# Optimization experiments

Measured on AMD Instinct MI355X. Metric: run time of the kernel, lower is better.

The kernel has to match this reference:

```python
import jax, jax.numpy as jnp
import numpy as np

N_HEAD = 16
NEG_BIG = 1e10

def setup_inputs() -> dict:
    key = jax.random.key(0)
    k1, k2, k3 = jax.random.split(key, 3)
    B, S, D = 2, 2048, 1024
    x = jax.random.normal(k1, (B, S, D), dtype=jnp.float32)
    c_attn_w = jax.random.normal(k2, (D, 3 * D), dtype=jnp.float32) * 0.02
    c_attn_b = jnp.zeros((3 * D,), dtype=jnp.float32)
    c_proj_w = jax.random.normal(k3, (D, D), dtype=jnp.float32) * 0.02
    c_proj_b = jnp.zeros((D,), dtype=jnp.float32)
    return {"x": x, "c_attn_w": c_attn_w, "c_attn_b": c_attn_b,
            "c_proj_w": c_proj_w, "c_proj_b": c_proj_b}

def reference(x, c_attn_w, c_attn_b, c_proj_w, c_proj_b):
    B, S, D = x.shape
    H = N_HEAD
    hd = D // H
    # Conv1D c_attn: x @ W + b -> (B, S, 3D)
    qkv = x @ c_attn_w + c_attn_b
    q, k, v = jnp.split(qkv, 3, axis=-1)
    # split heads -> (B, H, S, hd)
    q = q.reshape(B, S, H, hd).transpose(0, 2, 1, 3)
    k = k.reshape(B, S, H, hd).transpose(0, 2, 1, 3)
    v = v.reshape(B, S, H, hd).transpose(0, 2, 1, 3)
    # QK^T with scale (scale=True)
    w = jnp.einsum('bhqd,bhkd->bhqk', q, k) / jnp.sqrt(jnp.float32(hd))
    # additive/multiplicative causal mask, exactly as source: w*b - 1e10*(1-b)
    b = jnp.tril(jnp.ones((S, S), dtype=w.dtype))
    w = w * b - NEG_BIG * (1.0 - b)
    w = jax.nn.softmax(w, axis=-1)
    a = jnp.einsum('bhqk,bhkd->bhqd', w, v)
    # merge heads -> (B, S, D)
    a = a.transpose(0, 2, 1, 3).reshape(B, S, D)
    # Conv1D c_proj
    a = a @ c_proj_w + c_proj_b
    # present = stack(key (as (B,H,S,hd)), value)
    present = jnp.stack((k, v))
    return (a, present)
```

## Files before the change

### kernel.cpp

```cpp
#include <hip/hip_runtime.h>
#include <hip/hip_bf16.h>
#include <string.h>

#define BB 2
#define SS 2048
#define DD 1024
#define NH 16
#define TT (BB * SS)
#define N3 (3 * DD)
#define A_SIZE (TT * DD)
#define PRESENT_HALF (BB * NH * SS * 64)
#define C2Q 0.18033688011112043f

typedef __attribute__((ext_vector_type(8))) short short8;
typedef __attribute__((ext_vector_type(4))) float floatx4;
typedef __attribute__((ext_vector_type(8))) unsigned short ushort8;

__device__ __forceinline__ unsigned short f2bf(float f) {
    union { float f; unsigned u; } v; v.f = f;
    unsigned r = v.u + 0x7fffu + ((v.u >> 16) & 1u);
    return (unsigned short)(r >> 16);
}
__device__ __forceinline__ unsigned pack2bf(float a, float b) {
    __hip_bfloat162 h = __float22bfloat162_rn(float2{a, b});
    unsigned u; memcpy(&u, &h, 4); return u;
}
__device__ __forceinline__ float bf2f(unsigned short u) {
    union { unsigned u; float f; } v; v.u = ((unsigned)u) << 16; return v.f;
}

__device__ __forceinline__ void async16(const unsigned short* g, unsigned short* lds) {
    __builtin_amdgcn_global_load_lds(
        (const __attribute__((address_space(1))) unsigned int*)g,
        (__attribute__((address_space(3))) unsigned int*)lds,
        16, 0, 0);
}

__global__ __launch_bounds__(256) void cast_x_kernel(const float* __restrict__ src,
                                                     unsigned short* __restrict__ dst) {
    int i = (blockIdx.x * 256 + threadIdx.x) * 8;
    float4 a = *(const float4*)(src + i);
    float4 b = *(const float4*)(src + i + 4);
    ushort8 o;
    o[0] = f2bf(a.x); o[1] = f2bf(a.y); o[2] = f2bf(a.z); o[3] = f2bf(a.w);
    o[4] = f2bf(b.x); o[5] = f2bf(b.y); o[6] = f2bf(b.z); o[7] = f2bf(b.w);
    *(ushort8*)(dst + i) = o;
}

__global__ __launch_bounds__(256) void transpose_cast_kernel(const float* __restrict__ src,
                                                             unsigned short* __restrict__ dst,
                                                             int R, int C) {
    __shared__ float tile[32][33];
    int c0 = blockIdx.x * 32, r0 = blockIdx.y * 32;
    int tx = threadIdx.x, ty = threadIdx.y;
    for (int i = ty; i < 32; i += 8)
        tile[i][tx] = src[(size_t)(r0 + i) * C + c0 + tx];
    __syncthreads();
    for (int i = ty; i < 32; i += 8)
        dst[(size_t)(c0 + i) * R + r0 + tx] = f2bf(tile[tx][i]);
}

__global__ __launch_bounds__(256)
void vtrans_kernel(const unsigned short* __restrict__ qkv,
                   unsigned short* __restrict__ vT) {
    __shared__ unsigned short tile[64][72];
    int bh = blockIdx.x, st = blockIdx.y;
    int b = bh >> 4, h = bh & 15;
    int tid = threadIdx.x;
    int r = tid >> 2, c = (tid & 3) * 16;
    const unsigned short* src = qkv + ((size_t)(b * SS + st * 64 + r)) * 3072 + 2048 + h * 64 + c;
    *(int4*)(&tile[r][c])     = *(const int4*)(src);
    *(int4*)(&tile[r][c + 8]) = *(const int4*)(src + 8);
    __syncthreads();
    int d = tid >> 2, s0 = (tid & 3) * 16;
    unsigned short tmp[16];
    for (int e = 0; e < 16; ++e) tmp[e] = tile[s0 + e][d];
    unsigned short* dst = vT + ((size_t)bh * 64 + d) * SS + st * 64 + s0;
    *(int4*)(dst)     = *(const int4*)(tmp);
    *(int4*)(dst + 8) = *(const int4*)(tmp + 8);
}

__global__ __launch_bounds__(256)
void present_kernel(const unsigned short* __restrict__ qkvb, float* __restrict__ out) {
    size_t e = ((size_t)blockIdx.x * 256 + threadIdx.x) * 8;
    int d = (int)(e & 63);
    int s = (int)((e >> 6) & 2047);
    int h = (int)((e >> 17) & 15);
    int b = (int)((e >> 21) & 1);
    int half = (int)(e >> 22);
    const unsigned short* src = qkvb + ((size_t)(b * SS + s)) * 3072 + 1024 + half * 1024 + h * 64 + d;
    ushort8 u = *(const ushort8*)src;
    float* dst = out + A_SIZE + e;
    float4 f0 = {bf2f(u[0]), bf2f(u[1]), bf2f(u[2]), bf2f(u[3])};
    float4 f1 = {bf2f(u[4]), bf2f(u[5]), bf2f(u[6]), bf2f(u[7])};
    *(float4*)(dst) = f0;
    *(float4*)(dst + 4) = f1;
}

__global__ __launch_bounds__(256)
void gemm_kernel(const unsigned short* __restrict__ A,
                 const unsigned short* __restrict__ Bt,
                 const float* __restrict__ bias,
                 int mode,
                 unsigned short* __restrict__ out_bf,
                 float* __restrict__ out_f) {
    __shared__ unsigned short As[2][128][32];
    __shared__ unsigned short Bs[2][128][32];
    const int tid  = threadIdx.x;
    const int t0   = blockIdx.y * 128;
    const int n0   = blockIdx.x * 128;
    const int wave = tid >> 6, lane = tid & 63;
    const int wm = wave >> 1, wn = wave & 1;
    const int l15 = lane & 15, quad = lane >> 4;

    const int sr = lane >> 2;
    const int sc = (lane & 3) * 8;

    floatx4 acc[4][4];
    for (int i = 0; i < 4; ++i)
        for (int j = 0; j < 4; ++j)
            for (int e = 0; e < 4; ++e) acc[i][j][e] = 0.f;

    const unsigned short* gA = A  + (size_t)(t0 + wave * 32 + sr) * 1024 + sc;
    const unsigned short* gB = Bt + (size_t)(n0 + wave * 32 + sr) * 1024 + sc;

    async16(gA,             &As[0][wave * 32][0]);
    async16(gA + 16 * 1024, &As[0][wave * 32 + 16][0]);
    async16(gB,             &Bs[0][wave * 32][0]);
    async16(gB + 16 * 1024, &Bs[0][wave * 32 + 16][0]);

    for (int kt = 0; kt < 32; ++kt) {
        const int cur = kt & 1;
        __syncthreads();
        if (kt < 31) {
            const int k1 = (kt + 1) * 32;
            async16(gA + k1,             &As[cur ^ 1][wave * 32][0]);
            async16(gA + k1 + 16 * 1024, &As[cur ^ 1][wave * 32 + 16][0]);
            async16(gB + k1,             &Bs[cur ^ 1][wave * 32][0]);
            async16(gB + k1 + 16 * 1024, &Bs[cur ^ 1][wave * 32 + 16][0]);
        }
        short8 af[4], bfr[4];
        for (int mt = 0; mt < 4; ++mt)
            af[mt] = *(const short8*)(&As[cur][wm * 64 + mt * 16 + l15][quad * 8]);
        for (int nt = 0; nt < 4; ++nt)
            bfr[nt] = *(const short8*)(&Bs[cur][wn * 64 + nt * 16 + l15][quad * 8]);
        for (int mt = 0; mt < 4; ++mt)
            for (int nt = 0; nt < 4; ++nt)
                acc[mt][nt] = __builtin_amdgcn_mfma_f32_16x16x32_bf16(bfr[nt], af[mt], acc[mt][nt], 0, 0, 0);
    }

    const float qs = (mode == 0 && n0 < 1024) ? C2Q : 1.0f;
    for (int mt = 0; mt < 4; ++mt) {
        const int t = t0 + wm * 64 + mt * 16 + l15;
        if (mode == 0) {
            unsigned short* po = out_bf + (size_t)t * 3072 + n0 + wn * 64;
            for (int nt = 0; nt < 4; ++nt) {
                float4 b4 = *(const float4*)(bias + n0 + wn * 64 + nt * 16 + quad * 4);
                float v0 = (acc[mt][nt][0] + b4.x) * qs;
                float v1 = (acc[mt][nt][1] + b4.y) * qs;
                float v2 = (acc[mt][nt][2] + b4.z) * qs;
                float v3 = (acc[mt][nt][3] + b4.w) * qs;
                uint2 w = {pack2bf(v0, v1), pack2bf(v2, v3)};
                *(uint2*)(po + nt * 16 + quad * 4) = w;
            }
        } else {
            float* po = out_f + (size_t)t * 1024 + n0 + wn * 64;
            for (int nt = 0; nt < 4; ++nt) {
                float4 b4 = *(const float4*)(bias + n0 + wn * 64 + nt * 16 + quad * 4);
                float4 v = {acc[mt][nt][0] + b4.x, acc[mt][nt][1] + b4.y,
                            acc[mt][nt][2] + b4.z, acc[mt][nt][3] + b4.w};
                *(float4*)(po + nt * 16 + quad * 4) = v;
            }
        }
    }
}

__global__ __launch_bounds__(256)
void flash_kernel(const unsigned short* __restrict__ qkv,
                  const unsigned short* __restrict__ vT,
                  unsigned short* __restrict__ out) {
    __shared__ unsigned short Kt[2][64][72];
    __shared__ unsigned short Vt[2][64][72];
    __shared__ unsigned short Pt[4][16][72];

    const int bh = blockIdx.x;
    const int qt = 31 - blockIdx.y;
    const int b = bh >> 4, h = bh & 15;
    const int tid = threadIdx.x;
    const int wave = tid >> 6, lane = tid & 63;
    const int l15 = lane & 15, quad = lane >> 4;

    const size_t rowb = (size_t)b * SS;
    const int kcol = 1024 + h * 64;

    short8 bq0, bq1;
    {
        const unsigned short* qp = qkv + (rowb + qt * 64 + wave * 16 + l15) * 3072 + h * 64 + quad * 8;
        bq0 = *(const short8*)(qp);
        bq1 = *(const short8*)(qp + 32);
    }

    float l_i = 0.f;
    floatx4 o[4];
    for (int dt = 0; dt < 4; ++dt)
        for (int e = 0; e < 4; ++e) o[dt][e] = 0.f;

    const int qrow_l = wave * 16 + l15;

    const int rr = tid >> 3, seg = (tid & 7) * 8;
    const int vr = tid >> 2, vc = (tid & 3) * 16;
    const unsigned short* kb = qkv + rowb * 3072 + kcol;
    const unsigned short* vb = vT + (size_t)bh * 64 * SS;
    int4 ka0, ka1, va0, va1;

    #define PREF(j) { \
        const unsigned short* ks = kb + (size_t)((j) * 64 + rr) * 3072 + seg; \
        ka0 = *(const int4*)(ks); \
        ka1 = *(const int4*)(ks + 32 * 3072); \
        const unsigned short* vs = vb + (size_t)vr * SS + (j) * 64 + vc; \
        va0 = *(const int4*)(vs); \
        va1 = *(const int4*)(vs + 8); }
    #define STAGE(bf_) { \
        *(int4*)(&Kt[bf_][rr][seg])      = ka0; \
        *(int4*)(&Kt[bf_][rr + 32][seg]) = ka1; \
        *(int4*)(&Vt[bf_][vr][vc])       = va0; \
        *(int4*)(&Vt[bf_][vr][vc + 8])   = va1; }

    PREF(0);
    STAGE(0);
    if (qt > 0) PREF(1);

    for (int j = 0; j <= qt; ++j) {
        const int cur = j & 1;
        __syncthreads();
        if (j < qt) {
            STAGE(cur ^ 1);
            if (j + 2 <= qt) PREF(j + 2);
        }

        floatx4 sc[4];
        for (int nt = 0; nt < 4; ++nt)
            for (int e = 0; e < 4; ++e) sc[nt][e] = 0.f;
        for (int nt = 0; nt < 4; ++nt) {
            const unsigned short* kp = &Kt[cur][nt * 16 + l15][quad * 8];
            short8 ak0 = *(const short8*)(kp);
            short8 ak1 = *(const short8*)(kp + 32);
            sc[nt] = __builtin_amdgcn_mfma_f32_16x16x32_bf16(ak0, bq0, sc[nt], 0, 0, 0);
            sc[nt] = __builtin_amdgcn_mfma_f32_16x16x32_bf16(ak1, bq1, sc[nt], 0, 0, 0);
        }
        if (j == qt) {
            for (int nt = 0; nt < 4; ++nt)
                for (int r = 0; r < 4; ++r)
                    if (nt * 16 + quad * 4 + r > qrow_l) sc[nt][r] = -1.0e30f;
        }

        for (int nt = 0; nt < 4; ++nt)
            for (int r = 0; r < 4; ++r) {
                float p = __builtin_amdgcn_exp2f(sc[nt][r]);
                sc[nt][r] = p;
                l_i += p;
            }

        for (int nt = 0; nt < 4; ++nt) {
            uint2 w = {pack2bf(sc[nt][0], sc[nt][1]), pack2bf(sc[nt][2], sc[nt][3])};
            *(uint2*)(&Pt[wave][l15][nt * 16 + quad * 4]) = w;
        }
        asm volatile("s_waitcnt lgkmcnt(0)" ::: "memory");
        short8 bp0 = *(const short8*)(&Pt[wave][l15][quad * 8]);
        short8 bp1 = *(const short8*)(&Pt[wave][l15][32 + quad * 8]);
        for (int dt = 0; dt < 4; ++dt) {
            const unsigned short* vp = &Vt[cur][dt * 16 + l15][quad * 8];
            short8 av0 = *(const short8*)(vp);
            short8 av1 = *(const short8*)(vp + 32);
            o[dt] = __builtin_amdgcn_mfma_f32_16x16x32_bf16(av0, bp0, o[dt], 0, 0, 0);
            o[dt] = __builtin_amdgcn_mfma_f32_16x16x32_bf16(av1, bp1, o[dt], 0, 0, 0);
        }
    }
    #undef PREF
    #undef STAGE

    l_i += __shfl_xor(l_i, 16);
    l_i += __shfl_xor(l_i, 32);
    float inv = 1.f / l_i;
    const int qrow = qt * 64 + wave * 16 + l15;
    unsigned short* po = out + (rowb + qrow) * 1024 + h * 64;
    for (int dt = 0; dt < 4; ++dt) {
        uint2 w = {pack2bf(o[dt][0] * inv, o[dt][1] * inv),
                   pack2bf(o[dt][2] * inv, o[dt][3] * inv)};
        *(uint2*)(po + dt * 16 + quad * 4) = w;
    }
}

extern "C" void kernel_launch(void* const* d_in, const int* in_sizes, int n_in,
                              void* d_out, int out_size, void* d_ws, size_t ws_size,
                              hipStream_t stream) {
    const float* x        = (const float*)d_in[0];
    const float* c_attn_w = (const float*)d_in[1];
    const float* c_attn_b = (const float*)d_in[2];
    const float* c_proj_w = (const float*)d_in[3];
    const float* c_proj_b = (const float*)d_in[4];
    float* out = (float*)d_out;

    char* ws = (char*)d_ws;
    unsigned short* xb     = (unsigned short*)(ws);
    unsigned short* wqkvt  = (unsigned short*)(ws + 8388608);
    unsigned short* wprojt = (unsigned short*)(ws + 14680064);
    unsigned short* qkvb   = (unsigned short*)(ws + 16777216);
    unsigned short* aout   = (unsigned short*)(ws + 41943040);
    unsigned short* vT     = xb;

    cast_x_kernel<<<(TT * DD) / (256 * 8), 256, 0, stream>>>(x, xb);
    transpose_cast_kernel<<<dim3(N3 / 32, DD / 32), dim3(32, 8), 0, stream>>>(c_attn_w, wqkvt, DD, N3);
    transpose_cast_kernel<<<dim3(DD / 32, DD / 32), dim3(32, 8), 0, stream>>>(c_proj_w, wprojt, DD, DD);
    gemm_kernel<<<dim3(N3 / 128, TT / 128), 256, 0, stream>>>(xb, wqkvt, c_attn_b, 0, qkvb, out);
    present_kernel<<<(2 * PRESENT_HALF) / (256 * 8), 256, 0, stream>>>(qkvb, out);
    vtrans_kernel<<<dim3(32, 32), 256, 0, stream>>>(qkvb, vT);
    flash_kernel<<<dim3(32, 32), 256, 0, stream>>>(qkvb, vT, aout);
    gemm_kernel<<<dim3(DD / 128, TT / 128), 256, 0, stream>>>(aout, wprojt, c_proj_b, 1, nullptr, out);
}
```

Before: 217.7 us.

## Merge prep and KV kernels, pair query tiles in flash, narrow proj GEMM tiles

Three input-conversion kernels become a single prep launch, and the present-output and V-transpose kernels are fused so K and V are read once. The flash kernel now runs 512 threads covering two adjacent query tiles, which share each K/V tile load. Blocks are ordered to interleave light and heavy causal rows for load balance. The output projection GEMM uses 128x64 tiles so more blocks run in parallel. Fewer launches and less redundant K/V traffic come at the cost of idle waves in the paired flash blocks on the final tile.

```diff
diff --git a/kernel.cpp b/kernel.cpp
--- a/kernel.cpp
+++ b/kernel.cpp
@@ -36,23 +36,12 @@
         16, 0, 0);
 }
 
-__global__ __launch_bounds__(256) void cast_x_kernel(const float* __restrict__ src,
-                                                     unsigned short* __restrict__ dst) {
-    int i = (blockIdx.x * 256 + threadIdx.x) * 8;
-    float4 a = *(const float4*)(src + i);
-    float4 b = *(const float4*)(src + i + 4);
-    ushort8 o;
-    o[0] = f2bf(a.x); o[1] = f2bf(a.y); o[2] = f2bf(a.z); o[3] = f2bf(a.w);
-    o[4] = f2bf(b.x); o[5] = f2bf(b.y); o[6] = f2bf(b.z); o[7] = f2bf(b.w);
-    *(ushort8*)(dst + i) = o;
-}
-
-__global__ __launch_bounds__(256) void transpose_cast_kernel(const float* __restrict__ src,
-                                                             unsigned short* __restrict__ dst,
-                                                             int R, int C) {
+__device__ __forceinline__ void transpose_tile(const float* __restrict__ src,
+                                               unsigned short* __restrict__ dst,
+                                               int R, int C, int bx, int by, int tid) {
     __shared__ float tile[32][33];
-    int c0 = blockIdx.x * 32, r0 = blockIdx.y * 32;
-    int tx = threadIdx.x, ty = threadIdx.y;
+    int c0 = bx * 32, r0 = by * 32;
+    int tx = tid & 31, ty = tid >> 5;
     for (int i = ty; i < 32; i += 8)
         tile[i][tx] = src[(size_t)(r0 + i) * C + c0 + tx];
     __syncthreads();
@@ -61,16 +50,60 @@
 }
 
 __global__ __launch_bounds__(256)
-void vtrans_kernel(const unsigned short* __restrict__ qkv,
+void prep_kernel(const float* __restrict__ x,
+                 const float* __restrict__ wa,
+                 const float* __restrict__ wp,
+                 unsigned short* __restrict__ xb,
+                 unsigned short* __restrict__ wqkvt,
+                 unsigned short* __restrict__ wprojt) {
+    int bid = blockIdx.x, tid = threadIdx.x;
+    if (bid < 2048) {
+        int i = (bid * 256 + tid) * 8;
+        float4 a = *(const float4*)(x + i);
+        float4 b = *(const float4*)(x + i + 4);
+        ushort8 o;
+        o[0] = f2bf(a.x); o[1] = f2bf(a.y); o[2] = f2bf(a.z); o[3] = f2bf(a.w);
+        o[4] = f2bf(b.x); o[5] = f2bf(b.y); o[6] = f2bf(b.z); o[7] = f2bf(b.w);
+        *(ushort8*)(xb + i) = o;
+    } else if (bid < 2048 + 3072) {
+        int b2 = bid - 2048;
+        transpose_tile(wa, wqkvt, DD, N3, b2 % 96, b2 / 96, tid);
+    } else {
+        int b3 = bid - 5120;
+        transpose_tile(wp, wprojt, DD, DD, b3 & 31, b3 >> 5, tid);
+    }
+}
+
+__global__ __launch_bounds__(256)
+void kv_aux_kernel(const unsigned short* __restrict__ qkvb,
+                   float* __restrict__ out,
                    unsigned short* __restrict__ vT) {
     __shared__ unsigned short tile[64][72];
-    int bh = blockIdx.x, st = blockIdx.y;
-    int b = bh >> 4, h = bh & 15;
-    int tid = threadIdx.x;
-    int r = tid >> 2, c = (tid & 3) * 16;
-    const unsigned short* src = qkv + ((size_t)(b * SS + st * 64 + r)) * 3072 + 2048 + h * 64 + c;
-    *(int4*)(&tile[r][c])     = *(const int4*)(src);
-    *(int4*)(&tile[r][c + 8]) = *(const int4*)(src + 8);
+    const int bh = blockIdx.x, st = blockIdx.y;
+    const int b = bh >> 4, h = bh & 15;
+    const int tid = threadIdx.x;
+    const int r = tid >> 2, c = (tid & 3) * 16;
+    const int s = st * 64 + r;
+
+    const unsigned short* kp = qkvb + ((size_t)(b * SS + s)) * 3072 + 1024 + h * 64 + c;
+    ushort8 k0 = *(const ushort8*)(kp);
+    ushort8 k1 = *(const ushort8*)(kp + 8);
+    ushort8 v0 = *(const ushort8*)(kp + 1024);
+    ushort8 v1 = *(const ushort8*)(kp + 1032);
+
+    float* pk = out + A_SIZE + (((size_t)(b * NH + h) * SS + s) * 64 + c);
+    *(float4*)(pk)      = float4{bf2f(k0[0]), bf2f(k0[1]), bf2f(k0[2]), bf2f(k0[3])};
+    *(float4*)(pk + 4)  = float4{bf2f(k0[4]), bf2f(k0[5]), bf2f(k0[6]), bf2f(k0[7])};
+    *(float4*)(pk + 8)  = float4{bf2f(k1[0]), bf2f(k1[1]), bf2f(k1[2]), bf2f(k1[3])};
+    *(float4*)(pk + 12) = float4{bf2f(k1[4]), bf2f(k1[5]), bf2f(k1[6]), bf2f(k1[7])};
+    float* pv = pk + PRESENT_HALF;
+    *(float4*)(pv)      = float4{bf2f(v0[0]), bf2f(v0[1]), bf2f(v0[2]), bf2f(v0[3])};
+    *(float4*)(pv + 4)  = float4{bf2f(v0[4]), bf2f(v0[5]), bf2f(v0[6]), bf2f(v0[7])};
+    *(float4*)(pv + 8)  = float4{bf2f(v1[0]), bf2f(v1[1]), bf2f(v1[2]), bf2f(v1[3])};
+    *(float4*)(pv + 12) = float4{bf2f(v1[4]), bf2f(v1[5]), bf2f(v1[6]), bf2f(v1[7])};
+
+    *(ushort8*)(&tile[r][c])     = v0;
+    *(ushort8*)(&tile[r][c + 8]) = v1;
     __syncthreads();
     int d = tid >> 2, s0 = (tid & 3) * 16;
     unsigned short tmp[16];
@@ -81,29 +114,10 @@
 }
 
 __global__ __launch_bounds__(256)
-void present_kernel(const unsigned short* __restrict__ qkvb, float* __restrict__ out) {
-    size_t e = ((size_t)blockIdx.x * 256 + threadIdx.x) * 8;
-    int d = (int)(e & 63);
-    int s = (int)((e >> 6) & 2047);
-    int h = (int)((e >> 17) & 15);
-    int b = (int)((e >> 21) & 1);
-    int half = (int)(e >> 22);
-    const unsigned short* src = qkvb + ((size_t)(b * SS + s)) * 3072 + 1024 + half * 1024 + h * 64 + d;
-    ushort8 u = *(const ushort8*)src;
-    float* dst = out + A_SIZE + e;
-    float4 f0 = {bf2f(u[0]), bf2f(u[1]), bf2f(u[2]), bf2f(u[3])};
-    float4 f1 = {bf2f(u[4]), bf2f(u[5]), bf2f(u[6]), bf2f(u[7])};
-    *(float4*)(dst) = f0;
-    *(float4*)(dst + 4) = f1;
-}
-
-__global__ __launch_bounds__(256)
-void gemm_kernel(const unsigned short* __restrict__ A,
-                 const unsigned short* __restrict__ Bt,
-                 const float* __restrict__ bias,
-                 int mode,
-                 unsigned short* __restrict__ out_bf,
-                 float* __restrict__ out_f) {
+void gemm1_kernel(const unsigned short* __restrict__ A,
+                  const unsigned short* __restrict__ Bt,
+                  const float* __restrict__ bias,
+                  unsigned short* __restrict__ out_bf) {
     __shared__ unsigned short As[2][128][32];
     __shared__ unsigned short Bs[2][128][32];
     const int tid  = threadIdx.x;
@@ -112,9 +126,7 @@
     const int wave = tid >> 6, lane = tid & 63;
     const int wm = wave >> 1, wn = wave & 1;
     const int l15 = lane & 15, quad = lane >> 4;
-
-    const int sr = lane >> 2;
-    const int sc = (lane & 3) * 8;
+    const int sr = lane >> 2, sc = (lane & 3) * 8;
 
     floatx4 acc[4][4];
     for (int i = 0; i < 4; ++i)
@@ -149,53 +161,102 @@
                 acc[mt][nt] = __builtin_amdgcn_mfma_f32_16x16x32_bf16(bfr[nt], af[mt], acc[mt][nt], 0, 0, 0);
     }
 
-    const float qs = (mode == 0 && n0 < 1024) ? C2Q : 1.0f;
+    const float qs = (n0 < 1024) ? C2Q : 1.0f;
     for (int mt = 0; mt < 4; ++mt) {
         const int t = t0 + wm * 64 + mt * 16 + l15;
-        if (mode == 0) {
-            unsigned short* po = out_bf + (size_t)t * 3072 + n0 + wn * 64;
-            for (int nt = 0; nt < 4; ++nt) {
-                float4 b4 = *(const float4*)(bias + n0 + wn * 64 + nt * 16 + quad * 4);
-                float v0 = (acc[mt][nt][0] + b4.x) * qs;
-                float v1 = (acc[mt][nt][1] + b4.y) * qs;
-                float v2 = (acc[mt][nt][2] + b4.z) * qs;
-                float v3 = (acc[mt][nt][3] + b4.w) * qs;
-                uint2 w = {pack2bf(v0, v1), pack2bf(v2, v3)};
-                *(uint2*)(po + nt * 16 + quad * 4) = w;
-            }
-        } else {
-            float* po = out_f + (size_t)t * 1024 + n0 + wn * 64;
-            for (int nt = 0; nt < 4; ++nt) {
-                float4 b4 = *(const float4*)(bias + n0 + wn * 64 + nt * 16 + quad * 4);
-                float4 v = {acc[mt][nt][0] + b4.x, acc[mt][nt][1] + b4.y,
-                            acc[mt][nt][2] + b4.z, acc[mt][nt][3] + b4.w};
-                *(float4*)(po + nt * 16 + quad * 4) = v;
-            }
+        unsigned short* po = out_bf + (size_t)t * 3072 + n0 + wn * 64;
+        for (int nt = 0; nt < 4; ++nt) {
+            float4 b4 = *(const float4*)(bias + n0 + wn * 64 + nt * 16 + quad * 4);
+            uint2 w = {pack2bf((acc[mt][nt][0] + b4.x) * qs, (acc[mt][nt][1] + b4.y) * qs),
+                       pack2bf((acc[mt][nt][2] + b4.z) * qs, (acc[mt][nt][3] + b4.w) * qs)};
+            *(uint2*)(po + nt * 16 + quad * 4) = w;
         }
     }
 }
 
 __global__ __launch_bounds__(256)
+void gemm2_kernel(const unsigned short* __restrict__ A,
+                  const unsigned short* __restrict__ Bt,
+                  const float* __restrict__ bias,
+                  float* __restrict__ out_f) {
+    __shared__ unsigned short As[2][128][32];
+    __shared__ unsigned short Bs[2][64][32];
+    const int tid  = threadIdx.x;
+    const int t0   = blockIdx.y * 128;
+    const int n0   = blockIdx.x * 64;
+    const int wave = tid >> 6, lane = tid & 63;
+    const int wm = wave >> 1, wn = wave & 1;
+    const int l15 = lane & 15, quad = lane >> 4;
+    const int sr = lane >> 2, sc = (lane & 3) * 8;
+
+    floatx4 acc[4][2];
+    for (int i = 0; i < 4; ++i)
+        for (int j = 0; j < 2; ++j)
+            for (int e = 0; e < 4; ++e) acc[i][j][e] = 0.f;
+
+    const unsigned short* gA = A  + (size_t)(t0 + wave * 32 + sr) * 1024 + sc;
+    const unsigned short* gB = Bt + (size_t)(n0 + wave * 16 + sr) * 1024 + sc;
+
+    async16(gA,             &As[0][wave * 32][0]);
+    async16(gA + 16 * 1024, &As[0][wave * 32 + 16][0]);
+    async16(gB,             &Bs[0][wave * 16][0]);
+
+    for (int kt = 0; kt < 32; ++kt) {
+        const int cur = kt & 1;
+        __syncthreads();
+        if (kt < 31) {
+            const int k1 = (kt + 1) * 32;
+            async16(gA + k1,             &As[cur ^ 1][wave * 32][0]);
+            async16(gA + k1 + 16 * 1024, &As[cur ^ 1][wave * 32 + 16][0]);
+            async16(gB + k1,             &Bs[cur ^ 1][wave * 16][0]);
+        }
+        short8 af[4], bfr[2];
+        for (int mt = 0; mt < 4; ++mt)
+            af[mt] = *(const short8*)(&As[cur][wm * 64 + mt * 16 + l15][quad * 8]);
+        for (int nt = 0; nt < 2; ++nt)
+            bfr[nt] = *(const short8*)(&Bs[cur][wn * 32 + nt * 16 + l15][quad * 8]);
+        for (int mt = 0; mt < 4; ++mt)
+            for (int nt = 0; nt < 2; ++nt)
+                acc[mt][nt] = __builtin_amdgcn_mfma_f32_16x16x32_bf16(bfr[nt], af[mt], acc[mt][nt], 0, 0, 0);
+    }
+
+    for (int mt = 0; mt < 4; ++mt) {
+        const int t = t0 + wm * 64 + mt * 16 + l15;
+        float* po = out_f + (size_t)t * 1024 + n0 + wn * 32;
+        for (int nt = 0; nt < 2; ++nt) {
+            float4 b4 = *(const float4*)(bias + n0 + wn * 32 + nt * 16 + quad * 4);
+            float4 v = {acc[mt][nt][0] + b4.x, acc[mt][nt][1] + b4.y,
+                        acc[mt][nt][2] + b4.z, acc[mt][nt][3] + b4.w};
+            *(float4*)(po + nt * 16 + quad * 4) = v;
+        }
+    }
+}
+
+__global__ __launch_bounds__(512)
 void flash_kernel(const unsigned short* __restrict__ qkv,
                   const unsigned short* __restrict__ vT,
                   unsigned short* __restrict__ out) {
     __shared__ unsigned short Kt[2][64][72];
     __shared__ unsigned short Vt[2][64][72];
-    __shared__ unsigned short Pt[4][16][72];
+    __shared__ unsigned short Pt[8][16][72];
 
     const int bh = blockIdx.x;
-    const int qt = 31 - blockIdx.y;
+    const int yy = blockIdx.y;
+    const int qy = (yy & 1) ? (yy >> 1) : (15 - (yy >> 1));
     const int b = bh >> 4, h = bh & 15;
     const int tid = threadIdx.x;
     const int wave = tid >> 6, lane = tid & 63;
+    const int group = wave >> 2, w4 = wave & 3;
     const int l15 = lane & 15, quad = lane >> 4;
 
+    const int my_qt = 2 * qy + group;
+    const int jmax  = 2 * qy + 1;
+
     const size_t rowb = (size_t)b * SS;
-    const int kcol = 1024 + h * 64;
 
     short8 bq0, bq1;
     {
-        const unsigned short* qp = qkv + (rowb + qt * 64 + wave * 16 + l15) * 3072 + h * 64 + quad * 8;
+        const unsigned short* qp = qkv + (rowb + my_qt * 64 + w4 * 16 + l15) * 3072 + h * 64 + quad * 8;
         bq0 = *(const short8*)(qp);
         bq1 = *(const short8*)(qp + 32);
     }
@@ -205,38 +266,29 @@
     for (int dt = 0; dt < 4; ++dt)
         for (int e = 0; e < 4; ++e) o[dt][e] = 0.f;
 
-    const int qrow_l = wave * 16 + l15;
+    const int qrow_l = w4 * 16 + l15;
 
     const int rr = tid >> 3, seg = (tid & 7) * 8;
-    const int vr = tid >> 2, vc = (tid & 3) * 16;
-    const unsigned short* kb = qkv + rowb * 3072 + kcol;
+    const unsigned short* kb = qkv + rowb * 3072 + 1024 + h * 64;
     const unsigned short* vb = vT + (size_t)bh * 64 * SS;
-    int4 ka0, ka1, va0, va1;
-
-    #define PREF(j) { \
-        const unsigned short* ks = kb + (size_t)((j) * 64 + rr) * 3072 + seg; \
-        ka0 = *(const int4*)(ks); \
-        ka1 = *(const int4*)(ks + 32 * 3072); \
-        const unsigned short* vs = vb + (size_t)vr * SS + (j) * 64 + vc; \
-        va0 = *(const int4*)(vs); \
-        va1 = *(const int4*)(vs + 8); }
-    #define STAGE(bf_) { \
-        *(int4*)(&Kt[bf_][rr][seg])      = ka0; \
-        *(int4*)(&Kt[bf_][rr + 32][seg]) = ka1; \
-        *(int4*)(&Vt[bf_][vr][vc])       = va0; \
-        *(int4*)(&Vt[bf_][vr][vc + 8])   = va1; }
+    int4 ka, va;
+
+    #define PREF(j) { ka = *(const int4*)(kb + (size_t)((j) * 64 + rr) * 3072 + seg); \
+                      va = *(const int4*)(vb + (size_t)rr * SS + (j) * 64 + seg); }
+    #define STAGE(bf_) { *(int4*)(&Kt[bf_][rr][seg]) = ka; *(int4*)(&Vt[bf_][rr][seg]) = va; }
 
     PREF(0);
     STAGE(0);
-    if (qt > 0) PREF(1);
-
-    for (int j = 0; j <= qt; ++j) {
+    if (jmax > 0) PREF(1);
+
+    for (int j = 0; j <= jmax; ++j) {
         const int cur = j & 1;
         __syncthreads();
-        if (j < qt) {
+        if (j < jmax) {
             STAGE(cur ^ 1);
-            if (j + 2 <= qt) PREF(j + 2);
-        }
+            if (j + 2 <= jmax) PREF(j + 2);
+        }
+        if (j > my_qt) continue;
 
         floatx4 sc[4];
         for (int nt = 0; nt < 4; ++nt)
@@ -248,7 +300,7 @@
             sc[nt] = __builtin_amdgcn_mfma_f32_16x16x32_bf16(ak0, bq0, sc[nt], 0, 0, 0);
             sc[nt] = __builtin_amdgcn_mfma_f32_16x16x32_bf16(ak1, bq1, sc[nt], 0, 0, 0);
         }
-        if (j == qt) {
+        if (j == my_qt) {
             for (int nt = 0; nt < 4; ++nt)
                 for (int r = 0; r < 4; ++r)
                     if (nt * 16 + quad * 4 + r > qrow_l) sc[nt][r] = -1.0e30f;
@@ -282,7 +334,7 @@
     l_i += __shfl_xor(l_i, 16);
     l_i += __shfl_xor(l_i, 32);
     float inv = 1.f / l_i;
-    const int qrow = qt * 64 + wave * 16 + l15;
+    const int qrow = my_qt * 64 + w4 * 16 + l15;
     unsigned short* po = out + (rowb + qrow) * 1024 + h * 64;
     for (int dt = 0; dt < 4; ++dt) {
         uint2 w = {pack2bf(o[dt][0] * inv, o[dt][1] * inv),
@@ -309,12 +361,9 @@
     unsigned short* aout   = (unsigned short*)(ws + 41943040);
     unsigned short* vT     = xb;
 
-    cast_x_kernel<<<(TT * DD) / (256 * 8), 256, 0, stream>>>(x, xb);
-    transpose_cast_kernel<<<dim3(N3 / 32, DD / 32), dim3(32, 8), 0, stream>>>(c_attn_w, wqkvt, DD, N3);
-    transpose_cast_kernel<<<dim3(DD / 32, DD / 32), dim3(32, 8), 0, stream>>>(c_proj_w, wprojt, DD, DD);
-    gemm_kernel<<<dim3(N3 / 128, TT / 128), 256, 0, stream>>>(xb, wqkvt, c_attn_b, 0, qkvb, out);
-    present_kernel<<<(2 * PRESENT_HALF) / (256 * 8), 256, 0, stream>>>(qkvb, out);
-    vtrans_kernel<<<dim3(32, 32), 256, 0, stream>>>(qkvb, vT);
-    flash_kernel<<<dim3(32, 32), 256, 0, stream>>>(qkvb, vT, aout);
-    gemm_kernel<<<dim3(DD / 128, TT / 128), 256, 0, stream>>>(aout, wprojt, c_proj_b, 1, nullptr, out);
-}
+    prep_kernel<<<2048 + 3072 + 1024, 256, 0, stream>>>(x, c_attn_w, c_proj_w, xb, wqkvt, wprojt);
+    gemm1_kernel<<<dim3(N3 / 128, TT / 128), 256, 0, stream>>>(xb, wqkvt, c_attn_b, qkvb);
+    kv_aux_kernel<<<dim3(32, 32), 256, 0, stream>>>(qkvb, out, vT);
+    flash_kernel<<<dim3(32, 16), 512, 0, stream>>>(qkvb, vT, aout);
+    gemm2_kernel<<<dim3(DD / 64, TT / 128), 256, 0, stream>>>(aout, wprojt, c_proj_b, out);
+}
```

Result: no change. 219.9 us (+1.0%).
